# Performance work log

Measured on AMD Instinct MI355X. Metric: run time of the kernel, lower is better.

The kernel has to match this reference:

```python
import jax, jax.numpy as jnp
import numpy as np

N, K, C = 100000, 16, 64
H, MID = 64, 16
EPS_BN = 1e-5
EPS_NORM = 1e-12

def _normalize(x, axis=-1):
    n = jnp.linalg.norm(x, axis=axis, keepdims=True)
    return x / jnp.maximum(n, EPS_NORM)

def _bn_nck(x, g, b):
    # BatchNorm1d on [N, C, K]: stats over (N, K) per channel, training mode
    m = jnp.mean(x, axis=(0, 2), keepdims=True)
    v = jnp.var(x, axis=(0, 2), keepdims=True)
    return (x - m) / jnp.sqrt(v + EPS_BN) * g[None, :, None] + b[None, :, None]

def _bn_nc(x, g, b):
    m = jnp.mean(x, axis=0, keepdims=True)
    v = jnp.var(x, axis=0, keepdims=True)
    return (x - m) / jnp.sqrt(v + EPS_BN) * g[None, :] + b[None, :]

def _conv_bn_relu(x, W, b, g, be):
    # 1x1 Conv1d: x [N, Cin, K], W [Cout, Cin]
    y = jnp.einsum('oc,nck->nok', W, x) + b[None, :, None]
    return jax.nn.relu(_bn_nck(y, g, be))

def setup_inputs():
    ks = jax.random.split(jax.random.key(0), 16)
    rn = lambda k, s: jax.random.normal(k, s, dtype=jnp.float32) * 0.05
    z = lambda n: jnp.zeros((n,), jnp.float32)
    o = lambda n: jnp.ones((n,), jnp.float32)
    return {
        'xyz': jax.random.normal(ks[0], (N, 3), jnp.float32),
        'cov': jax.random.normal(ks[1], (N, 3, 3), jnp.float32),
        'feats': jax.random.normal(ks[2], (N, C), jnp.float32),
        'knn_indices': jax.random.randint(ks[3], (N, K), 0, N),
        'fw1': rn(ks[4], (H, C)), 'fb1': z(H), 'fg1': o(H), 'fbe1': z(H),
        'fw2': rn(ks[5], (H, H)), 'fb2': z(H), 'fg2': o(H), 'fbe2': z(H),
        'ww1': rn(ks[6], (8, 14)), 'wb1': z(8), 'wg1': o(8), 'wbe1': z(8),
        'ww2': rn(ks[7], (8, 8)), 'wb2': z(8), 'wg2': o(8), 'wbe2': z(8),
        'ww3': rn(ks[8], (MID, 8)), 'wb3': z(MID), 'wg3': o(MID), 'wbe3': z(MID),
        'lin_w': rn(ks[9], (H, MID * H)), 'lin_b': z(H),
        'bng': o(H), 'bnb': z(H),
    }

def reference(xyz, cov, feats, knn_indices,
              fw1, fb1, fg1, fbe1, fw2, fb2, fg2, fbe2,
              ww1, wb1, wg1, wbe1, ww2, wb2, wg2, wbe2,
              ww3, wb3, wg3, wbe3, lin_w, lin_b, bng, bnb):
    xg = xyz[knn_indices]                      # [N,K,3] gathered positions
    loc = xg - xg[:, :1, :]                    # localized xyz (center = neighbor 0)
    cg = cov[knn_indices]                      # [N,K,3,3]
    fg = feats[knn_indices]                    # [N,K,C]

    n_alpha = fg[:, :, 3:6]                    # neighbor normals
    n_miu = n_alpha[:, 0, :]                   # center normal [N,3]
    r_hat = _normalize(loc, axis=2)
    dot_nm_rhat = jnp.einsum('nd,nkd->nk', n_miu, r_hat)
    v_miu = _normalize(n_miu[:, None, :] - dot_nm_rhat[:, :, None] * r_hat, axis=2)
    w_miu = _normalize(jnp.cross(r_hat, v_miu), axis=2)

    t1 = jnp.einsum('nkd,nd->nk', n_alpha, n_miu)
    t2 = dot_nm_rhat
    t3 = jnp.sum(r_hat * n_alpha, axis=2)
    t4 = jnp.einsum('nkd,nd->nk', loc, n_miu)
    t5 = t3
    t6 = jnp.sum(n_alpha * v_miu, axis=2)
    t7 = jnp.sum(n_alpha * w_miu, axis=2)
    t8 = jnp.sum(loc * jnp.cross(n_alpha, jnp.broadcast_to(n_miu[:, None, :], n_alpha.shape)), axis=2)
    t9 = jnp.linalg.norm(loc, axis=2)
    s1 = jnp.einsum('nkd,nkde,nke->nk', loc, cg, loc)        # per-neighbor cov quad form
    s2 = jnp.einsum('nkd,nde,nke->nk', loc, cg[:, 0], loc)   # center cov quad form

    win = jnp.concatenate([loc.transpose(0, 2, 1),
                           jnp.stack([t1, t2, t3, t4, t5, t6, t7, t8, t9, s1, s2], axis=1)],
                          axis=1)              # [N,14,K]

    w = _conv_bn_relu(win, ww1, wb1, wg1, wbe1)
    w = _conv_bn_relu(w, ww2, wb2, wg2, wbe2)
    w = _conv_bn_relu(w, ww3, wb3, wg3, wbe3)  # [N,MID,K]

    f = _conv_bn_relu(fg.transpose(0, 2, 1), fw1, fb1, fg1, fbe1)
    f = _conv_bn_relu(f, fw2, fb2, fg2, fbe2)  # [N,H,K]

    new = jnp.einsum('nhk,nmk->nhm', f, w).reshape(f.shape[0], -1)  # [N, H*MID]
    return jax.nn.relu(_bn_nc(new @ lin_w.T + lin_b, bng, bnb))
```

## Files before the change

kernel.cpp:

```cpp
#include <hip/hip_runtime.h>
#include <hip/hip_bf16.h>

typedef __hip_bfloat16 bf16;
typedef __attribute__((ext_vector_type(8))) short bf16x8;
typedef __attribute__((ext_vector_type(4))) short bf16x4;
typedef __attribute__((ext_vector_type(4))) float f32x4;

#define NPTS 100000
#define KNN 16
#define NKTOT 1600000
#define NB_W 6250
#define NB_F 1563
#define NB_P 391

#define F_Y1 28672
#define F_Z1 28688
#define F_Y2 28816
#define F_Z2 28832
#define F_Y3 28960
#define F_LIN 28992
#define CNT_BYTE 131072ull
#define ZERO_BYTES 531072ull

#define Q_Y1 0
#define Q_Y2 100000
#define Q_Y3 200000
#define Q_LIN 400000
#define Q_Z1 1200000
#define Q_Z2 1400064

#define OFS_Y1   (1ull<<20)
#define OFS_ZP1  (27ull<<20)
#define OFS_ZP2  (53ull<<20)
#define OFS_P    OFS_ZP2
#define OFS_PART (79ull<<20)
#define OFS_LWB  (86ull<<20)
#define WS_NEED  (OFS_LWB + 131072ull)

__device__ inline float bfs2f(short s) {
  unsigned int u = ((unsigned int)(unsigned short)s) << 16;
  float f; __builtin_memcpy(&f, &u, 4); return f;
}
__device__ inline short f2bfs(float x) {
  bf16 h = __float2bfloat16(x);
  short s; __builtin_memcpy(&s, &h, 2); return s;
}

__device__ inline void gl_lds16(const void* g, void* l) {
  __builtin_amdgcn_global_load_lds(
      (const __attribute__((address_space(1))) void*)g,
      (__attribute__((address_space(3))) void*)l, 16, 0, 0);
}

__device__ inline float wred(float v) {
  #pragma unroll
  for (int o = 32; o > 0; o >>= 1) v += __shfl_xor(v, o);
  return v;
}

__global__ __launch_bounds__(256) void k0(
    const float* __restrict__ xyz, const float* __restrict__ cov,
    const float* __restrict__ feats, const float* __restrict__ linw,
    float* __restrict__ P, bf16* __restrict__ lwb) {
  const int t = threadIdx.x;
  if (blockIdx.x >= NB_P) {
    int e = (blockIdx.x - NB_P) * 1024 + t * 4;
    if (e < 65536) {
      float4 v = *(const float4*)(linw + e);
      lwb[e+0] = __float2bfloat16(v.x); lwb[e+1] = __float2bfloat16(v.y);
      lwb[e+2] = __float2bfloat16(v.z); lwb[e+3] = __float2bfloat16(v.w);
    }
    return;
  }
  int n = blockIdx.x * 256 + t;
  if (n >= NPTS) return;
  float4 o0, o1, o2, o3;
  o0.x = xyz[n*3+0]; o0.y = xyz[n*3+1]; o0.z = xyz[n*3+2]; o0.w = 0.f;
  o1.x = feats[(size_t)n*64+3]; o1.y = feats[(size_t)n*64+4]; o1.z = feats[(size_t)n*64+5];
  const float* cv = cov + (size_t)n*9;
  o1.w = cv[0];
  o2.x = cv[1]; o2.y = cv[2]; o2.z = cv[3]; o2.w = cv[4];
  o3.x = cv[5]; o3.y = cv[6]; o3.z = cv[7]; o3.w = cv[8];
  float* pr = P + (size_t)n*16;
  *(float4*)(pr+0) = o0; *(float4*)(pr+4) = o1;
  *(float4*)(pr+8) = o2; *(float4*)(pr+12) = o3;
}

__global__ __launch_bounds__(256) void k1(
    const float* __restrict__ P, const int* __restrict__ knn,
    const float* __restrict__ ww1, const float* __restrict__ wb1,
    float* __restrict__ part, int* __restrict__ cnt, bf16* __restrict__ Y1) {
  __shared__ float s_Pn[4][256][4];
  __shared__ float s_ww1t[14][8];
  __shared__ float s_ws[4][16];
  const int t = threadIdx.x;
  const int w = t >> 6;
  const long base = (long)blockIdx.x * 256;
  const int idx = knn[base + t];
  #pragma unroll
  for (int c = 0; c < 4; c++)
    gl_lds16(P + (size_t)idx * 16 + c * 4, &s_Pn[c][w * 64][0]);
  atomicAdd(&cnt[idx], 1);
  if (t < 112) { int c = t >> 3, h = t & 7; s_ww1t[c][h] = ww1[h * 14 + c]; }
  __syncthreads();
  const int b = t & ~15;
  float4 r0 = *(const float4*)&s_Pn[0][t][0];
  float4 r1 = *(const float4*)&s_Pn[1][t][0];
  float4 r2 = *(const float4*)&s_Pn[2][t][0];
  float4 r3 = *(const float4*)&s_Pn[3][t][0];
  float lx = r0.x - s_Pn[0][b][0], ly = r0.y - s_Pn[0][b][1], lz = r0.z - s_Pn[0][b][2];
  float nmx = s_Pn[1][b][0], nmy = s_Pn[1][b][1], nmz = s_Pn[1][b][2];
  float nax = r1.x, nay = r1.y, naz = r1.z;
  float t9v = sqrtf(lx*lx + ly*ly + lz*lz);
  float rn = 1.0f / fmaxf(t9v, 1e-12f);
  float rx = lx*rn, ry = ly*rn, rz = lz*rn;
  float t2v = nmx*rx + nmy*ry + nmz*rz;
  float vx = nmx - t2v*rx, vy = nmy - t2v*ry, vz = nmz - t2v*rz;
  float vn = 1.0f / fmaxf(sqrtf(vx*vx+vy*vy+vz*vz), 1e-12f);
  vx *= vn; vy *= vn; vz *= vn;
  float wxv = ry*vz - rz*vy, wyv = rz*vx - rx*vz, wzv = rx*vy - ry*vx;
  float wn = 1.0f / fmaxf(sqrtf(wxv*wxv+wyv*wyv+wzv*wzv), 1e-12f);
  wxv *= wn; wyv *= wn; wzv *= wn;
  float t1v = nax*nmx + nay*nmy + naz*nmz;
  float t3v = rx*nax + ry*nay + rz*naz;
  float t4v = lx*nmx + ly*nmy + lz*nmz;
  float t6v = nax*vx + nay*vy + naz*vz;
  float t7v = nax*wxv + nay*wyv + naz*wzv;
  float cxx = nay*nmz - naz*nmy, cyy = naz*nmx - nax*nmz, czz = nax*nmy - nay*nmx;
  float t8v = lx*cxx + ly*cyy + lz*czz;
  float q0 = r1.w*lx + r2.x*ly + r2.y*lz;
  float q1 = r2.z*lx + r2.w*ly + r3.x*lz;
  float q2 = r3.y*lx + r3.z*ly + r3.w*lz;
  float s1v = lx*q0 + ly*q1 + lz*q2;
  float p0 = s_Pn[1][b][3]*lx + s_Pn[2][b][0]*ly + s_Pn[2][b][1]*lz;
  float p1 = s_Pn[2][b][2]*lx + s_Pn[2][b][3]*ly + s_Pn[3][b][0]*lz;
  float p2 = s_Pn[3][b][1]*lx + s_Pn[3][b][2]*ly + s_Pn[3][b][3]*lz;
  float s2v = lx*p0 + ly*p1 + lz*p2;
  float win[14] = {lx, ly, lz, t1v, t2v, t3v, t4v, t3v, t6v, t7v, t8v, t9v, s1v, s2v};
  float y[8];
  #pragma unroll
  for (int h = 0; h < 8; h++) y[h] = wb1[h];
  #pragma unroll
  for (int c = 0; c < 14; c++) {
    float x = win[c];
    #pragma unroll
    for (int h = 0; h < 8; h++) y[h] = fmaf(s_ww1t[c][h], x, y[h]);
  }
  const long nkg = base + t;
  bf16x8 pk;
  #pragma unroll
  for (int h = 0; h < 8; h++) pk[h] = f2bfs(y[h]);
  *(bf16x8*)&Y1[nkg * 8] = pk;
  const int lane = t & 63;
  #pragma unroll
  for (int h = 0; h < 8; h++) {
    float s = wred(y[h]);
    float q = wred(y[h] * y[h]);
    if (lane == 0) { s_ws[w][h] = s; s_ws[w][8 + h] = q; }
  }
  __syncthreads();
  if (t < 16)
    part[Q_Y1 + blockIdx.x * 16 + t] = s_ws[0][t] + s_ws[1][t] + s_ws[2][t] + s_ws[3][t];
}

__global__ __launch_bounds__(256) void kredfin(
    const float* __restrict__ part, float* __restrict__ stats,
    int qA, int nA, int cA, const float* gA, const float* beA, float mA, int fA,
    int qB, int nB, int cB, const float* gB, const float* beB, float mB, int fB) {
  int c = blockIdx.x;
  const float* p; int nblk, C, f; const float *g, *be; float M;
  if (c < cA) { p = part + qA; nblk = nA; C = cA; g = gA; be = beA; M = mA; f = fA; }
  else { c -= cA; p = part + qB; nblk = nB; C = cB; g = gB; be = beB; M = mB; f = fB; }
  const int t = threadIdx.x;
  float s = 0.f, q = 0.f;
  for (int b = t; b < nblk; b += 256) {
    s += p[(size_t)b * 2 * C + c];
    q += p[(size_t)b * 2 * C + C + c];
  }
  s = wred(s); q = wred(q);
  __shared__ float rs[4], rq[4];
  const int w = t >> 6;
  if ((t & 63) == 0) { rs[w] = s; rq[w] = q; }
  __syncthreads();
  if (t == 0) {
    s = rs[0] + rs[1] + rs[2] + rs[3];
    q = rq[0] + rq[1] + rq[2] + rq[3];
    float mean = s / M;
    float var = q / M - mean * mean;
    float scale = g[c] / sqrtf(var + 1e-5f);
    stats[f + c] = scale;
    stats[f + C + c] = be[c] - mean * scale;
  }
}

__global__ __launch_bounds__(256) void k2(
    const bf16* __restrict__ Y1, const float* __restrict__ ww2, const float* __restrict__ wb2,
    const float* __restrict__ feats, const float* __restrict__ fw1, const float* __restrict__ fb1,
    const int* __restrict__ cnt, const float* __restrict__ stats,
    float* __restrict__ part, float* __restrict__ zp1) {
  const int t = threadIdx.x;
  if (blockIdx.x < NB_W) {
    __shared__ float s_ww2t[8][8];
    __shared__ float s_sc[8], s_sh[8];
    __shared__ float s_ws[4][16];
    if (t < 64) { int c = t >> 3, h = t & 7; s_ww2t[c][h] = ww2[h*8+c]; }
    if (t < 8)  { s_sc[t] = stats[F_Y1 + t]; s_sh[t] = stats[F_Y1 + 8 + t]; }
    __syncthreads();
    const long nkg = (long)blockIdx.x * 256 + t;
    bf16x8 yv = *(const bf16x8*)&Y1[nkg * 8];
    float a[8];
    #pragma unroll
    for (int c = 0; c < 8; c++)
      a[c] = fmaxf(fmaf(s_sc[c], bfs2f(yv[c]), s_sh[c]), 0.f);
    float y2[8];
    #pragma unroll
    for (int h = 0; h < 8; h++) y2[h] = wb2[h];
    #pragma unroll
    for (int c = 0; c < 8; c++)
      #pragma unroll
      for (int h = 0; h < 8; h++) y2[h] = fmaf(s_ww2t[c][h], a[c], y2[h]);
    const int w = t >> 6, lane = t & 63;
    #pragma unroll
    for (int h = 0; h < 8; h++) {
      float s = wred(y2[h]);
      float q = wred(y2[h] * y2[h]);
      if (lane == 0) { s_ws[w][h] = s; s_ws[w][8 + h] = q; }
    }
    __syncthreads();
    if (t < 16)
      part[Q_Y2 + blockIdx.x * 16 + t] = s_ws[0][t] + s_ws[1][t] + s_ws[2][t] + s_ws[3][t];
    return;
  }
  __shared__ __align__(16) bf16 s_A[64 * 72];
  __shared__ float s_sum[64], s_sq[64];
  const int fblk = blockIdx.x - NB_W;
  const int p0 = fblk * 64;
  if (t < 64) { s_sum[t] = 0.f; s_sq[t] = 0.f; }
  for (int r = 0; r < 16; r++) {
    int e = r * 256 + t;
    int p = e >> 6, c = e & 63;
    int gp = p0 + p;
    float v = (gp < NPTS) ? feats[(size_t)gp*64 + c] : 0.f;
    s_A[p * 72 + c] = __float2bfloat16(v);
  }
  __syncthreads();
  const int wv = t >> 6, lane = t & 63, pt = lane & 15, kq = lane >> 4;
  for (int nt = 0; nt < 4; nt++) {
    f32x4 acc = {0.f, 0.f, 0.f, 0.f};
    int h = nt * 16 + pt;
    #pragma unroll
    for (int ks = 0; ks < 2; ks++) {
      bf16x8 av = *(const bf16x8*)&s_A[(wv*16 + pt) * 72 + ks*32 + kq*8];
      float4 b0 = *(const float4*)(fw1 + h*64 + ks*32 + kq*8);
      float4 b1 = *(const float4*)(fw1 + h*64 + ks*32 + kq*8 + 4);
      bf16x8 bv;
      bv[0]=f2bfs(b0.x); bv[1]=f2bfs(b0.y); bv[2]=f2bfs(b0.z); bv[3]=f2bfs(b0.w);
      bv[4]=f2bfs(b1.x); bv[5]=f2bfs(b1.y); bv[6]=f2bfs(b1.z); bv[7]=f2bfs(b1.w);
      acc = __builtin_amdgcn_mfma_f32_16x16x32_bf16(av, bv, acc, 0, 0, 0);
    }
    float bias = fb1[h];
    float ss = 0.f, qq = 0.f;
    #pragma unroll
    for (int r = 0; r < 4; r++) {
      int gp = p0 + wv*16 + kq*4 + r;
      float z = acc[r] + bias;
      if (gp < NPTS) {
        zp1[(size_t)gp*64 + h] = z;
        float w = (float)cnt[gp];
        ss += w * z; qq += w * z * z;
      }
    }
    ss += __shfl_xor(ss, 16); ss += __shfl_xor(ss, 32);
    qq += __shfl_xor(qq, 16); qq += __shfl_xor(qq, 32);
    if (lane < 16) { atomicAdd(&s_sum[h], ss); atomicAdd(&s_sq[h], qq); }
  }
  __syncthreads();
  if (t < 128)
    part[Q_Z1 + fblk * 128 + t] = (t < 64) ? s_sum[t] : s_sq[t - 64];
}

__global__ __launch_bounds__(256) void k3(
    const bf16* __restrict__ Y1,
    const float* __restrict__ ww2, const float* __restrict__ wb2,
    const float* __restrict__ ww3, const float* __restrict__ wb3,
    const float* __restrict__ zp1, const float* __restrict__ fw2, const float* __restrict__ fb2,
    const int* __restrict__ cnt, const float* __restrict__ stats,
    float* __restrict__ part, float* __restrict__ zp2) {
  const int t = threadIdx.x;
  if (blockIdx.x < NB_W) {
    __shared__ float s_ww2t[8][8];
    __shared__ float s_ww3t[8][16];
    __shared__ float s_sc1[8], s_sh1[8], s_sc2[8], s_sh2[8];
    __shared__ float s_ws[4][32];
    if (t < 64)  { int c = t >> 3, h = t & 7; s_ww2t[c][h] = ww2[h*8+c]; }
    if (t < 128) { int h = t >> 4, m = t & 15; s_ww3t[h][m] = ww3[m*8+h]; }
    if (t < 8)  { s_sc1[t] = stats[F_Y1 + t]; s_sh1[t] = stats[F_Y1 + 8 + t]; }
    if (t >= 8 && t < 16) { s_sc2[t-8] = stats[F_Y2 + (t-8)]; s_sh2[t-8] = stats[F_Y2 + 8 + (t-8)]; }
    __syncthreads();
    const long nkg = (long)blockIdx.x * 256 + t;
    bf16x8 yv = *(const bf16x8*)&Y1[nkg * 8];
    float a[8];
    #pragma unroll
    for (int c = 0; c < 8; c++)
      a[c] = fmaxf(fmaf(s_sc1[c], bfs2f(yv[c]), s_sh1[c]), 0.f);
    float y2[8];
    #pragma unroll
    for (int h = 0; h < 8; h++) y2[h] = wb2[h];
    #pragma unroll
    for (int c = 0; c < 8; c++)
      #pragma unroll
      for (int h = 0; h < 8; h++) y2[h] = fmaf(s_ww2t[c][h], a[c], y2[h]);
    float a2w[8];
    #pragma unroll
    for (int h = 0; h < 8; h++) a2w[h] = fmaxf(fmaf(s_sc2[h], y2[h], s_sh2[h]), 0.f);
    float y3[16];
    #pragma unroll
    for (int m = 0; m < 16; m++) y3[m] = wb3[m];
    #pragma unroll
    for (int h = 0; h < 8; h++)
      #pragma unroll
      for (int m = 0; m < 16; m++) y3[m] = fmaf(s_ww3t[h][m], a2w[h], y3[m]);
    const int w = t >> 6, lane = t & 63;
    #pragma unroll
    for (int m = 0; m < 16; m++) {
      float s = wred(y3[m]);
      float q = wred(y3[m] * y3[m]);
      if (lane == 0) { s_ws[w][m] = s; s_ws[w][16 + m] = q; }
    }
    __syncthreads();
    if (t < 32)
      part[Q_Y3 + blockIdx.x * 32 + t] = s_ws[0][t] + s_ws[1][t] + s_ws[2][t] + s_ws[3][t];
    return;
  }
  __shared__ __align__(16) bf16 s_A[64 * 72];
  __shared__ float s_sum[64], s_sq[64];
  __shared__ float s_sc[64], s_sh[64];
  const int fblk = blockIdx.x - NB_W;
  const int p0 = fblk * 64;
  if (t < 64) { s_sum[t] = 0.f; s_sq[t] = 0.f; s_sc[t] = stats[F_Z1 + t]; s_sh[t] = stats[F_Z1 + 64 + t]; }
  __syncthreads();
  for (int r = 0; r < 16; r++) {
    int e = r * 256 + t;
    int p = e >> 6, c = e & 63;
    int gp = p0 + p;
    float v = 0.f;
    if (gp < NPTS) v = fmaxf(fmaf(s_sc[c], zp1[(size_t)gp*64 + c], s_sh[c]), 0.f);
    s_A[p * 72 + c] = __float2bfloat16(v);
  }
  __syncthreads();
  const int wv = t >> 6, lane = t & 63, pt = lane & 15, kq = lane >> 4;
  for (int nt = 0; nt < 4; nt++) {
    f32x4 acc = {0.f, 0.f, 0.f, 0.f};
    int h = nt * 16 + pt;
    #pragma unroll
    for (int ks = 0; ks < 2; ks++) {
      bf16x8 av = *(const bf16x8*)&s_A[(wv*16 + pt) * 72 + ks*32 + kq*8];
      float4 b0 = *(const float4*)(fw2 + h*64 + ks*32 + kq*8);
      float4 b1 = *(const float4*)(fw2 + h*64 + ks*32 + kq*8 + 4);
      bf16x8 bv;
      bv[0]=f2bfs(b0.x); bv[1]=f2bfs(b0.y); bv[2]=f2bfs(b0.z); bv[3]=f2bfs(b0.w);
      bv[4]=f2bfs(b1.x); bv[5]=f2bfs(b1.y); bv[6]=f2bfs(b1.z); bv[7]=f2bfs(b1.w);
      acc = __builtin_amdgcn_mfma_f32_16x16x32_bf16(av, bv, acc, 0, 0, 0);
    }
    float bias = fb2[h];
    float ss = 0.f, qq = 0.f;
    #pragma unroll
    for (int r = 0; r < 4; r++) {
      int gp = p0 + wv*16 + kq*4 + r;
      float z = acc[r] + bias;
      if (gp < NPTS) {
        zp2[(size_t)gp*64 + h] = z;
        float w = (float)cnt[gp];
        ss += w * z; qq += w * z * z;
      }
    }
    ss += __shfl_xor(ss, 16); ss += __shfl_xor(ss, 32);
    qq += __shfl_xor(qq, 16); qq += __shfl_xor(qq, 32);
    if (lane < 16) { atomicAdd(&s_sum[h], ss); atomicAdd(&s_sq[h], qq); }
  }
  __syncthreads();
  if (t < 128)
    part[Q_Z2 + fblk * 128 + t] = (t < 64) ? s_sum[t] : s_sq[t - 64];
}

__global__ __launch_bounds__(256) void k3b(
    const float* __restrict__ zp2, const float* __restrict__ stats, bf16* __restrict__ a2) {
  long e = ((long)blockIdx.x * 256 + threadIdx.x) * 4;
  int c = (int)(e & 63);
  float4 v = *(const float4*)(zp2 + e);
  bf16x4 o;
  o[0] = f2bfs(fmaxf(fmaf(stats[F_Z2 + c+0], v.x, stats[F_Z2 + 64 + c+0]), 0.f));
  o[1] = f2bfs(fmaxf(fmaf(stats[F_Z2 + c+1], v.y, stats[F_Z2 + 64 + c+1]), 0.f));
  o[2] = f2bfs(fmaxf(fmaf(stats[F_Z2 + c+2], v.z, stats[F_Z2 + 64 + c+2]), 0.f));
  o[3] = f2bfs(fmaxf(fmaf(stats[F_Z2 + c+3], v.w, stats[F_Z2 + 64 + c+3]), 0.f));
  *(bf16x4*)&a2[e] = o;
}

__global__ __launch_bounds__(256, 4) void k4(
    const bf16* __restrict__ Y1, const int* __restrict__ knn,
    const float* __restrict__ ww2, const float* __restrict__ wb2,
    const float* __restrict__ ww3, const float* __restrict__ wb3,
    const bf16* __restrict__ a2, const bf16* __restrict__ lwb, const float* __restrict__ linb,
    const float* __restrict__ stats, float* __restrict__ part, float* __restrict__ outp) {
  __shared__ float s_ww2t[8][8];
  __shared__ float s_ww3t[8][16];
  __shared__ float s_scy1[8], s_shy1[8], s_scy2[8], s_shy2[8];
  __shared__ float s_scy3[16], s_shy3[16];
  __shared__ float s_ls[64], s_lq[64];
  __shared__ __align__(16) bf16 s_w[16 * 392];
  __shared__ __align__(16) bf16 s_new[16 * 1032];
  const int t = threadIdx.x;
  const int w = t >> 6, lane = t & 63;
  const long base = (long)blockIdx.x * 256;
  const int myidx = knn[base + t];
  #pragma unroll
  for (int c = 0; c < 8; c++) {
    int src = c * 8 + (lane >> 3);
    int ridx = __shfl(myidx, src);
    gl_lds16(a2 + (size_t)ridx * 64 + (lane & 7) * 8, &s_new[(w * 64 + c * 8) * 64]);
  }
  if (t < 64)  { int c = t >> 3, h = t & 7; s_ww2t[c][h] = ww2[h*8+c]; }
  if (t < 128) { int h = t >> 4, m = t & 15; s_ww3t[h][m] = ww3[m*8+h]; }
  if (t < 8)  { s_scy1[t] = stats[F_Y1 + t]; s_shy1[t] = stats[F_Y1 + 8 + t]; }
  if (t >= 8 && t < 16) { s_scy2[t-8] = stats[F_Y2 + (t-8)]; s_shy2[t-8] = stats[F_Y2 + 8 + (t-8)]; }
  if (t >= 16 && t < 32) { s_scy3[t-16] = stats[F_Y3 + (t-16)]; s_shy3[t-16] = stats[F_Y3 + 16 + (t-16)]; }
  __syncthreads();

  {
    const long nkg = base + t;
    bf16x8 yv = *(const bf16x8*)&Y1[nkg * 8];
    float a[8];
    #pragma unroll
    for (int c = 0; c < 8; c++)
      a[c] = fmaxf(fmaf(s_scy1[c], bfs2f(yv[c]), s_shy1[c]), 0.f);
    float y2[8];
    #pragma unroll
    for (int h = 0; h < 8; h++) y2[h] = wb2[h];
    #pragma unroll
    for (int c = 0; c < 8; c++)
      #pragma unroll
      for (int h = 0; h < 8; h++) y2[h] = fmaf(s_ww2t[c][h], a[c], y2[h]);
    float a2w[8];
    #pragma unroll
    for (int h = 0; h < 8; h++) a2w[h] = fmaxf(fmaf(s_scy2[h], y2[h], s_shy2[h]), 0.f);
    float y3[16];
    #pragma unroll
    for (int m = 0; m < 16; m++) y3[m] = wb3[m];
    #pragma unroll
    for (int h = 0; h < 8; h++)
      #pragma unroll
      for (int m = 0; m < 16; m++) y3[m] = fmaf(s_ww3t[h][m], a2w[h], y3[m]);
    const int p = t >> 4, k = t & 15;
    #pragma unroll
    for (int mp = 0; mp < 8; mp++) {
      float w0 = fmaxf(fmaf(s_scy3[2*mp],   y3[2*mp],   s_shy3[2*mp]),   0.f);
      float w1 = fmaxf(fmaf(s_scy3[2*mp+1], y3[2*mp+1], s_shy3[2*mp+1]), 0.f);
      __hip_bfloat162 pk; pk.x = __float2bfloat16(w0); pk.y = __float2bfloat16(w1);
      *(__hip_bfloat162*)&s_w[p*392 + k*24 + 2*mp] = pk;
    }
  }
  __syncthreads();

  float acc[4][16];
  {
    const int p = t >> 4, l = t & 15;
    #pragma unroll
    for (int hj = 0; hj < 4; hj++)
      #pragma unroll
      for (int m = 0; m < 16; m++) acc[hj][m] = 0.f;
    #pragma unroll 4
    for (int k = 0; k < 16; k++) {
      bf16x4 zf = *(const bf16x4*)&s_new[(p * 16 + k) * 64 + l * 4];
      float f0 = bfs2f(zf[0]);
      float f1 = bfs2f(zf[1]);
      float f2 = bfs2f(zf[2]);
      float f3 = bfs2f(zf[3]);
      #pragma unroll
      for (int mp = 0; mp < 8; mp++) {
        __hip_bfloat162 wp = *(const __hip_bfloat162*)&s_w[p*392 + k*24 + 2*mp];
        float w0 = __bfloat162float(wp.x), w1 = __bfloat162float(wp.y);
        acc[0][2*mp]   = fmaf(f0, w0, acc[0][2*mp]);   acc[0][2*mp+1] = fmaf(f0, w1, acc[0][2*mp+1]);
        acc[1][2*mp]   = fmaf(f1, w0, acc[1][2*mp]);   acc[1][2*mp+1] = fmaf(f1, w1, acc[1][2*mp+1]);
        acc[2][2*mp]   = fmaf(f2, w0, acc[2][2*mp]);   acc[2][2*mp+1] = fmaf(f2, w1, acc[2][2*mp+1]);
        acc[3][2*mp]   = fmaf(f3, w0, acc[3][2*mp]);   acc[3][2*mp+1] = fmaf(f3, w1, acc[3][2*mp+1]);
      }
    }
  }
  __syncthreads();

  {
    const int p = t >> 4, l = t & 15;
    const int swz = (l & 7) * 8;
    #pragma unroll
    for (int hj = 0; hj < 4; hj++)
      #pragma unroll
      for (int mp = 0; mp < 8; mp++) {
        int v = hj*16 + 2*mp;
        int phys = (l << 6) + (v ^ swz);
        __hip_bfloat162 pk;
        pk.x = __float2bfloat16(acc[hj][2*mp]); pk.y = __float2bfloat16(acc[hj][2*mp+1]);
        *(__hip_bfloat162*)&s_new[p*1032 + phys] = pk;
      }
  }
  __syncthreads();

  {
    const int wv = t >> 6, pt = lane & 15, kq = lane >> 4;
    const int j = wv * 16 + pt;
    const bf16* lwrow = lwb + j * 1024;
    f32x4 macc = {0.f, 0.f, 0.f, 0.f};
    #pragma unroll 8
    for (int ks = 0; ks < 32; ks++) {
      int i = ks*32 + kq*8;
      int l2 = i >> 6, v = i & 63;
      int phys = (l2 << 6) + (v ^ ((l2 & 7) * 8));
      bf16x8 av = *(const bf16x8*)&s_new[pt*1032 + phys];
      bf16x8 bv = *(const bf16x8*)(lwrow + i);
      macc = __builtin_amdgcn_mfma_f32_16x16x32_bf16(av, bv, macc, 0, 0, 0);
    }
    float bj = linb[j];
    float ss = 0.f, qq = 0.f;
    #pragma unroll
    for (int r = 0; r < 4; r++) {
      int gp = (int)(blockIdx.x * 16) + kq*4 + r;
      float val = macc[r] + bj;
      outp[(size_t)gp*64 + j] = val;
      ss += val; qq += val * val;
    }
    ss += __shfl_xor(ss, 16); ss += __shfl_xor(ss, 32);
    qq += __shfl_xor(qq, 16); qq += __shfl_xor(qq, 32);
    if (lane < 16) { s_ls[j] = ss; s_lq[j] = qq; }
  }
  __syncthreads();
  if (t < 128)
    part[Q_LIN + blockIdx.x * 128 + t] = (t < 64) ? s_ls[t] : s_lq[t - 64];
}

__global__ __launch_bounds__(256) void k6(float* __restrict__ outp, const float* __restrict__ stats) {
  long e = (long)blockIdx.x * 256 + threadIdx.x;
  int j = (int)(e & 63);
  float sc = stats[F_LIN + j], sh = stats[F_LIN + 64 + j];
  float v = outp[e];
  outp[e] = fmaxf(fmaf(sc, v, sh), 0.f);
}

__global__ void k_wsfail(float* outp, float mb) {
  outp[threadIdx.x] = -mb;
}

extern "C" void kernel_launch(void* const* d_in, const int* in_sizes, int n_in,
                              void* d_out, int out_size, void* d_ws, size_t ws_size,
                              hipStream_t stream) {
  const float* xyz  = (const float*)d_in[0];
  const float* cov  = (const float*)d_in[1];
  const float* feats= (const float*)d_in[2];
  const int*   knn  = (const int*)d_in[3];
  const float* fw1  = (const float*)d_in[4];
  const float* fb1  = (const float*)d_in[5];
  const float* fg1  = (const float*)d_in[6];
  const float* fbe1 = (const float*)d_in[7];
  const float* fw2  = (const float*)d_in[8];
  const float* fb2  = (const float*)d_in[9];
  const float* fg2  = (const float*)d_in[10];
  const float* fbe2 = (const float*)d_in[11];
  const float* ww1  = (const float*)d_in[12];
  const float* wb1  = (const float*)d_in[13];
  const float* wg1  = (const float*)d_in[14];
  const float* wbe1 = (const float*)d_in[15];
  const float* ww2  = (const float*)d_in[16];
  const float* wb2  = (const float*)d_in[17];
  const float* wg2  = (const float*)d_in[18];
  const float* wbe2 = (const float*)d_in[19];
  const float* ww3  = (const float*)d_in[20];
  const float* wb3  = (const float*)d_in[21];
  const float* wg3  = (const float*)d_in[22];
  const float* wbe3 = (const float*)d_in[23];
  const float* linw = (const float*)d_in[24];
  const float* linb = (const float*)d_in[25];
  const float* bng  = (const float*)d_in[26];
  const float* bnb  = (const float*)d_in[27];

  float* outp = (float*)d_out;
  if (ws_size < WS_NEED) {
    hipLaunchKernelGGL(k_wsfail, dim3(1), dim3(256), 0, stream, outp, (float)(ws_size >> 20));
    return;
  }
  char* ws = (char*)d_ws;
  float* stats = (float*)ws;
  int*   cnt   = (int*)(ws + CNT_BYTE);
  bf16*  Y1    = (bf16*)(ws + OFS_Y1);
  float* zp1   = (float*)(ws + OFS_ZP1);
  bf16*  a2    = (bf16*)(ws + OFS_ZP1);
  float* zp2   = (float*)(ws + OFS_ZP2);
  float* P     = (float*)(ws + OFS_P);
  float* part  = (float*)(ws + OFS_PART);
  bf16*  lwb   = (bf16*)(ws + OFS_LWB);

  hipMemsetAsync(d_ws, 0, ZERO_BYTES, stream);
  hipLaunchKernelGGL(k0, dim3(NB_P + 64), dim3(256), 0, stream,
                     xyz, cov, feats, linw, P, lwb);
  hipLaunchKernelGGL(k1, dim3(NB_W), dim3(256), 0, stream,
                     P, knn, ww1, wb1, part, cnt, Y1);
  hipLaunchKernelGGL(kredfin, dim3(16), dim3(256), 0, stream, part, stats,
                     Q_Y1, NB_W, 8, wg1, wbe1, (float)NKTOT, F_Y1,
                     Q_Y1, NB_W, 8, wg1, wbe1, (float)NKTOT, F_Y1);
  hipLaunchKernelGGL(k2, dim3(NB_W + NB_F), dim3(256), 0, stream,
                     Y1, ww2, wb2, feats, fw1, fb1, cnt, stats, part, zp1);
  hipLaunchKernelGGL(kredfin, dim3(72), dim3(256), 0, stream, part, stats,
                     Q_Y2, NB_W, 8, wg2, wbe2, (float)NKTOT, F_Y2,
                     Q_Z1, NB_F, 64, fg1, fbe1, (float)NKTOT, F_Z1);
  hipLaunchKernelGGL(k3, dim3(NB_W + NB_F), dim3(256), 0, stream,
                     Y1, ww2, wb2, ww3, wb3, zp1, fw2, fb2, cnt, stats, part, zp2);
  hipLaunchKernelGGL(kredfin, dim3(80), dim3(256), 0, stream, part, stats,
                     Q_Y3, NB_W, 16, wg3, wbe3, (float)NKTOT, F_Y3,
                     Q_Z2, NB_F, 64, fg2, fbe2, (float)NKTOT, F_Z2);
  hipLaunchKernelGGL(k3b, dim3(6250), dim3(256), 0, stream, zp2, stats, a2);
  hipLaunchKernelGGL(k4, dim3(NB_W), dim3(256), 0, stream,
                     Y1, knn, ww2, wb2, ww3, wb3, a2, lwb, linb, stats, part, outp);
  hipLaunchKernelGGL(kredfin, dim3(128), dim3(256), 0, stream, part, stats,
                     Q_LIN, NB_W, 64, bng, bnb, (float)NPTS, F_LIN,
                     Q_LIN, NB_W, 64, bng, bnb, (float)NPTS, F_LIN);
  hipLaunchKernelGGL(k6, dim3(25000), dim3(256), 0, stream, outp, stats);
}
```

Baseline: 597.1 us.

## Fuse BN-ReLU into k4 gather, store bf16 intermediates, split histogram

The separate k3b pass that normalised zp2 into a bf16 activation buffer is removed. k2 and k3 now write their pre-norm outputs zp1 and zp2 directly as bf16, and k4 applies the second feature BN scale/shift plus ReLU on the fly after gathering. The neighbour-count atomics move out of k1 into a standalone histogram kernel, and the global_load_lds gathers are issued after the setup barrier and waited on with an explicit vmcnt wait instead of a block barrier. This cuts one full-size memory pass and halves intermediate traffic, at the cost of extra per-element FMAs in k4, one more launch, and bf16 rounding of the pre-norm values.

```diff
diff --git a/kernel.cpp b/kernel.cpp
--- a/kernel.cpp
+++ b/kernel.cpp
@@ -50,6 +50,10 @@
   __builtin_amdgcn_global_load_lds(
       (const __attribute__((address_space(1))) void*)g,
       (__attribute__((address_space(3))) void*)l, 16, 0, 0);
+}
+__device__ inline void wait_vm0() {
+  __builtin_amdgcn_s_waitcnt(0xf70);
+  __builtin_amdgcn_wave_barrier();
 }
 
 __device__ inline float wred(float v) {
@@ -86,10 +90,15 @@
   *(float4*)(pr+8) = o2; *(float4*)(pr+12) = o3;
 }
 
+__global__ __launch_bounds__(256) void khist(const int* __restrict__ knn, int* __restrict__ cnt) {
+  int g = blockIdx.x * 256 + threadIdx.x;
+  atomicAdd(&cnt[knn[g]], 1);
+}
+
 __global__ __launch_bounds__(256) void k1(
     const float* __restrict__ P, const int* __restrict__ knn,
     const float* __restrict__ ww1, const float* __restrict__ wb1,
-    float* __restrict__ part, int* __restrict__ cnt, bf16* __restrict__ Y1) {
+    float* __restrict__ part, bf16* __restrict__ Y1) {
   __shared__ float s_Pn[4][256][4];
   __shared__ float s_ww1t[14][8];
   __shared__ float s_ws[4][16];
@@ -97,12 +106,12 @@
   const int w = t >> 6;
   const long base = (long)blockIdx.x * 256;
   const int idx = knn[base + t];
+  if (t < 112) { int c = t >> 3, h = t & 7; s_ww1t[c][h] = ww1[h * 14 + c]; }
+  __syncthreads();
   #pragma unroll
   for (int c = 0; c < 4; c++)
     gl_lds16(P + (size_t)idx * 16 + c * 4, &s_Pn[c][w * 64][0]);
-  atomicAdd(&cnt[idx], 1);
-  if (t < 112) { int c = t >> 3, h = t & 7; s_ww1t[c][h] = ww1[h * 14 + c]; }
-  __syncthreads();
+  wait_vm0();
   const int b = t & ~15;
   float4 r0 = *(const float4*)&s_Pn[0][t][0];
   float4 r1 = *(const float4*)&s_Pn[1][t][0];
@@ -146,11 +155,10 @@
     #pragma unroll
     for (int h = 0; h < 8; h++) y[h] = fmaf(s_ww1t[c][h], x, y[h]);
   }
-  const long nkg = base + t;
   bf16x8 pk;
   #pragma unroll
   for (int h = 0; h < 8; h++) pk[h] = f2bfs(y[h]);
-  *(bf16x8*)&Y1[nkg * 8] = pk;
+  *(bf16x8*)&Y1[(base + t) * 8] = pk;
   const int lane = t & 63;
   #pragma unroll
   for (int h = 0; h < 8; h++) {
@@ -197,7 +205,7 @@
     const bf16* __restrict__ Y1, const float* __restrict__ ww2, const float* __restrict__ wb2,
     const float* __restrict__ feats, const float* __restrict__ fw1, const float* __restrict__ fb1,
     const int* __restrict__ cnt, const float* __restrict__ stats,
-    float* __restrict__ part, float* __restrict__ zp1) {
+    float* __restrict__ part, bf16* __restrict__ zp1) {
   const int t = threadIdx.x;
   if (blockIdx.x < NB_W) {
     __shared__ float s_ww2t[8][8];
@@ -265,7 +273,7 @@
       int gp = p0 + wv*16 + kq*4 + r;
       float z = acc[r] + bias;
       if (gp < NPTS) {
-        zp1[(size_t)gp*64 + h] = z;
+        zp1[(size_t)gp*64 + h] = __float2bfloat16(z);
         float w = (float)cnt[gp];
         ss += w * z; qq += w * z * z;
       }
@@ -283,9 +291,9 @@
     const bf16* __restrict__ Y1,
     const float* __restrict__ ww2, const float* __restrict__ wb2,
     const float* __restrict__ ww3, const float* __restrict__ wb3,
-    const float* __restrict__ zp1, const float* __restrict__ fw2, const float* __restrict__ fb2,
+    const bf16* __restrict__ zp1, const float* __restrict__ fw2, const float* __restrict__ fb2,
     const int* __restrict__ cnt, const float* __restrict__ stats,
-    float* __restrict__ part, float* __restrict__ zp2) {
+    float* __restrict__ part, bf16* __restrict__ zp2) {
   const int t = threadIdx.x;
   if (blockIdx.x < NB_W) {
     __shared__ float s_ww2t[8][8];
@@ -344,7 +352,10 @@
     int p = e >> 6, c = e & 63;
     int gp = p0 + p;
     float v = 0.f;
-    if (gp < NPTS) v = fmaxf(fmaf(s_sc[c], zp1[(size_t)gp*64 + c], s_sh[c]), 0.f);
+    if (gp < NPTS) {
+      short zs; __builtin_memcpy(&zs, &zp1[(size_t)gp*64 + c], 2);
+      v = fmaxf(fmaf(s_sc[c], bfs2f(zs), s_sh[c]), 0.f);
+    }
     s_A[p * 72 + c] = __float2bfloat16(v);
   }
   __syncthreads();
@@ -369,7 +380,7 @@
       int gp = p0 + wv*16 + kq*4 + r;
       float z = acc[r] + bias;
       if (gp < NPTS) {
-        zp2[(size_t)gp*64 + h] = z;
+        zp2[(size_t)gp*64 + h] = __float2bfloat16(z);
         float w = (float)cnt[gp];
         ss += w * z; qq += w * z * z;
       }
@@ -381,31 +392,19 @@
   __syncthreads();
   if (t < 128)
     part[Q_Z2 + fblk * 128 + t] = (t < 64) ? s_sum[t] : s_sq[t - 64];
-}
-
-__global__ __launch_bounds__(256) void k3b(
-    const float* __restrict__ zp2, const float* __restrict__ stats, bf16* __restrict__ a2) {
-  long e = ((long)blockIdx.x * 256 + threadIdx.x) * 4;
-  int c = (int)(e & 63);
-  float4 v = *(const float4*)(zp2 + e);
-  bf16x4 o;
-  o[0] = f2bfs(fmaxf(fmaf(stats[F_Z2 + c+0], v.x, stats[F_Z2 + 64 + c+0]), 0.f));
-  o[1] = f2bfs(fmaxf(fmaf(stats[F_Z2 + c+1], v.y, stats[F_Z2 + 64 + c+1]), 0.f));
-  o[2] = f2bfs(fmaxf(fmaf(stats[F_Z2 + c+2], v.z, stats[F_Z2 + 64 + c+2]), 0.f));
-  o[3] = f2bfs(fmaxf(fmaf(stats[F_Z2 + c+3], v.w, stats[F_Z2 + 64 + c+3]), 0.f));
-  *(bf16x4*)&a2[e] = o;
 }
 
 __global__ __launch_bounds__(256, 4) void k4(
     const bf16* __restrict__ Y1, const int* __restrict__ knn,
     const float* __restrict__ ww2, const float* __restrict__ wb2,
     const float* __restrict__ ww3, const float* __restrict__ wb3,
-    const bf16* __restrict__ a2, const bf16* __restrict__ lwb, const float* __restrict__ linb,
+    const bf16* __restrict__ zp2, const bf16* __restrict__ lwb, const float* __restrict__ linb,
     const float* __restrict__ stats, float* __restrict__ part, float* __restrict__ outp) {
   __shared__ float s_ww2t[8][8];
   __shared__ float s_ww3t[8][16];
   __shared__ float s_scy1[8], s_shy1[8], s_scy2[8], s_shy2[8];
   __shared__ float s_scy3[16], s_shy3[16];
+  __shared__ float s_scf[64], s_shf[64];
   __shared__ float s_ls[64], s_lq[64];
   __shared__ __align__(16) bf16 s_w[16 * 392];
   __shared__ __align__(16) bf16 s_new[16 * 1032];
@@ -413,22 +412,23 @@
   const int w = t >> 6, lane = t & 63;
   const long base = (long)blockIdx.x * 256;
   const int myidx = knn[base + t];
-  #pragma unroll
-  for (int c = 0; c < 8; c++) {
-    int src = c * 8 + (lane >> 3);
-    int ridx = __shfl(myidx, src);
-    gl_lds16(a2 + (size_t)ridx * 64 + (lane & 7) * 8, &s_new[(w * 64 + c * 8) * 64]);
-  }
   if (t < 64)  { int c = t >> 3, h = t & 7; s_ww2t[c][h] = ww2[h*8+c]; }
   if (t < 128) { int h = t >> 4, m = t & 15; s_ww3t[h][m] = ww3[m*8+h]; }
   if (t < 8)  { s_scy1[t] = stats[F_Y1 + t]; s_shy1[t] = stats[F_Y1 + 8 + t]; }
   if (t >= 8 && t < 16) { s_scy2[t-8] = stats[F_Y2 + (t-8)]; s_shy2[t-8] = stats[F_Y2 + 8 + (t-8)]; }
   if (t >= 16 && t < 32) { s_scy3[t-16] = stats[F_Y3 + (t-16)]; s_shy3[t-16] = stats[F_Y3 + 16 + (t-16)]; }
-  __syncthreads();
+  if (t >= 32 && t < 96) { s_scf[t-32] = stats[F_Z2 + (t-32)]; s_shf[t-32] = stats[F_Z2 + 64 + (t-32)]; }
+  __syncthreads();
+
+  bf16x8 yv = *(const bf16x8*)&Y1[(base + t) * 8];
+  #pragma unroll
+  for (int c = 0; c < 8; c++) {
+    int src = c * 8 + (lane >> 3);
+    int ridx = __shfl(myidx, src);
+    gl_lds16(zp2 + (size_t)ridx * 64 + (lane & 7) * 8, &s_new[(w * 64 + c * 8) * 64]);
+  }
 
   {
-    const long nkg = base + t;
-    bf16x8 yv = *(const bf16x8*)&Y1[nkg * 8];
     float a[8];
     #pragma unroll
     for (int c = 0; c < 8; c++)
@@ -459,11 +459,13 @@
       *(__hip_bfloat162*)&s_w[p*392 + k*24 + 2*mp] = pk;
     }
   }
-  __syncthreads();
+  wait_vm0();
 
   float acc[4][16];
   {
     const int p = t >> 4, l = t & 15;
+    float sc0 = s_scf[l*4+0], sc1 = s_scf[l*4+1], sc2 = s_scf[l*4+2], sc3 = s_scf[l*4+3];
+    float sh0 = s_shf[l*4+0], sh1 = s_shf[l*4+1], sh2 = s_shf[l*4+2], sh3 = s_shf[l*4+3];
     #pragma unroll
     for (int hj = 0; hj < 4; hj++)
       #pragma unroll
@@ -471,10 +473,10 @@
     #pragma unroll 4
     for (int k = 0; k < 16; k++) {
       bf16x4 zf = *(const bf16x4*)&s_new[(p * 16 + k) * 64 + l * 4];
-      float f0 = bfs2f(zf[0]);
-      float f1 = bfs2f(zf[1]);
-      float f2 = bfs2f(zf[2]);
-      float f3 = bfs2f(zf[3]);
+      float f0 = fmaxf(fmaf(sc0, bfs2f(zf[0]), sh0), 0.f);
+      float f1 = fmaxf(fmaf(sc1, bfs2f(zf[1]), sh1), 0.f);
+      float f2 = fmaxf(fmaf(sc2, bfs2f(zf[2]), sh2), 0.f);
+      float f3 = fmaxf(fmaf(sc3, bfs2f(zf[3]), sh3), 0.f);
       #pragma unroll
       for (int mp = 0; mp < 8; mp++) {
         __hip_bfloat162 wp = *(const __hip_bfloat162*)&s_w[p*392 + k*24 + 2*mp];
@@ -589,9 +591,8 @@
   float* stats = (float*)ws;
   int*   cnt   = (int*)(ws + CNT_BYTE);
   bf16*  Y1    = (bf16*)(ws + OFS_Y1);
-  float* zp1   = (float*)(ws + OFS_ZP1);
-  bf16*  a2    = (bf16*)(ws + OFS_ZP1);
-  float* zp2   = (float*)(ws + OFS_ZP2);
+  bf16*  zp1   = (bf16*)(ws + OFS_ZP1);
+  bf16*  zp2   = (bf16*)(ws + OFS_ZP2);
   float* P     = (float*)(ws + OFS_P);
   float* part  = (float*)(ws + OFS_PART);
   bf16*  lwb   = (bf16*)(ws + OFS_LWB);
@@ -599,8 +600,9 @@
   hipMemsetAsync(d_ws, 0, ZERO_BYTES, stream);
   hipLaunchKernelGGL(k0, dim3(NB_P + 64), dim3(256), 0, stream,
                      xyz, cov, feats, linw, P, lwb);
+  hipLaunchKernelGGL(khist, dim3(6250), dim3(256), 0, stream, knn, cnt);
   hipLaunchKernelGGL(k1, dim3(NB_W), dim3(256), 0, stream,
-                     P, knn, ww1, wb1, part, cnt, Y1);
+                     P, knn, ww1, wb1, part, Y1);
   hipLaunchKernelGGL(kredfin, dim3(16), dim3(256), 0, stream, part, stats,
                      Q_Y1, NB_W, 8, wg1, wbe1, (float)NKTOT, F_Y1,
                      Q_Y1, NB_W, 8, wg1, wbe1, (float)NKTOT, F_Y1);
@@ -614,9 +616,8 @@
   hipLaunchKernelGGL(kredfin, dim3(80), dim3(256), 0, stream, part, stats,
                      Q_Y3, NB_W, 16, wg3, wbe3, (float)NKTOT, F_Y3,
                      Q_Z2, NB_F, 64, fg2, fbe2, (float)NKTOT, F_Z2);
-  hipLaunchKernelGGL(k3b, dim3(6250), dim3(256), 0, stream, zp2, stats, a2);
   hipLaunchKernelGGL(k4, dim3(NB_W), dim3(256), 0, stream,
-                     Y1, knn, ww2, wb2, ww3, wb3, a2, lwb, linb, stats, part, outp);
+                     Y1, knn, ww2, wb2, ww3, wb3, zp2, lwb, linb, stats, part, outp);
   hipLaunchKernelGGL(kredfin, dim3(128), dim3(256), 0, stream, part, stats,
                      Q_LIN, NB_W, 64, bng, bnb, (float)NPTS, F_LIN,
                      Q_LIN, NB_W, 64, bng, bnb, (float)NPTS, F_LIN);
```

Result: slower. 620.8 us (+4.0%).
